# Kernel optimization log

Hardware: AMD Instinct MI355X
Metric: run time of the kernel (lower is better)

## Reference

```python
import jax, jax.numpy as jnp
import numpy as np

SELECT_SIZE = 64
SM_SCALE = 0.07216878364870322  # 192 ** -0.5
V_HEAD_DIM = 128


def setup_inputs() -> dict:
    key = jax.random.key(0)
    k1, k2, k3, k4 = jax.random.split(key, 4)
    B, S, Hq, G, TOPK = 4, 2048, 16, 4, 16
    T = B * S
    NB = S // SELECT_SIZE  # 32 blocks per sequence
    q = jax.random.normal(k1, (T, Hq, 192), dtype=jnp.float32)
    k = jax.random.normal(k2, (T, Hq, 192), dtype=jnp.float32)
    v = jax.random.normal(k3, (T, Hq, V_HEAD_DIM), dtype=jnp.float32)
    idx = jax.random.randint(k4, (T, G, TOPK), 0, NB, dtype=jnp.int32)
    # guarantee block 0 is always selected so every causal row has >=1 valid key
    idx = idx.at[..., 0].set(0)
    idx = jnp.sort(idx, axis=-1)
    return {"q": q, "k": k, "v": v, "selected_indices": idx,
            "batch_size": B, "seq_len": S}


def reference(q, k, v, selected_indices, batch_size, seq_len):
    B, S = batch_size, seq_len
    Hq = q.shape[1]
    G = selected_indices.shape[1]
    Hg = Hq // G  # query heads per selection-score group
    nb = (S + SELECT_SIZE - 1) // SELECT_SIZE
    dv = v.shape[-1]

    # un-ragged: B equal-length sequences
    qg = q.reshape(B, S, G, Hg, -1)
    kg = k.reshape(B, S, G, Hg, -1)
    vg = v.reshape(B, S, G, Hg, -1)
    idx = selected_indices.reshape(B, S, G, -1)

    # which KV blocks are selected for each (query position, group): [B,S,G,nb]
    allowed_blk = (idx[..., None] == jnp.arange(nb, dtype=idx.dtype)).any(axis=-2)
    blk_of_pos = jnp.arange(S) // SELECT_SIZE
    pos_ok = allowed_blk[..., blk_of_pos]  # [B, Tq, G, Skv]
    causal = jnp.arange(S)[:, None] >= jnp.arange(S)[None, :]
    mask = pos_ok & causal[None, :, None, :]          # [B, Tq, G, Skv]
    mask = mask.transpose(0, 2, 1, 3)[:, :, None]      # [B, G, 1, Tq, Skv]

    scores = jnp.einsum('btghd,bsghd->bghts', qg, kg) * SM_SCALE
    scores = jnp.where(mask, scores, jnp.float32(-1e30))
    attn = jax.nn.softmax(scores, axis=-1)
    o = jnp.einsum('bghts,bsghd->btghd', attn, vg)
    return o.reshape(B * S, Hq * dv)
```

## Files before the change

### kernel.cpp

```cpp
#include <hip/hip_runtime.h>


typedef __attribute__((ext_vector_type(8))) _Float16 half8;
typedef __attribute__((ext_vector_type(4))) float f32x4;
typedef __attribute__((ext_vector_type(4))) unsigned int u32x4;

__device__ __forceinline__ half8 cvt8s(const float4* p, float s) {
  float4 a = p[0], b = p[1];
  half8 r;
  r[0] = (_Float16)(a.x * s); r[1] = (_Float16)(a.y * s);
  r[2] = (_Float16)(a.z * s); r[3] = (_Float16)(a.w * s);
  r[4] = (_Float16)(b.x * s); r[5] = (_Float16)(b.y * s);
  r[6] = (_Float16)(b.z * s); r[7] = (_Float16)(b.w * s);
  return r;
}

__device__ __forceinline__ void async16(const void* g, void* l) {
  __builtin_amdgcn_global_load_lds(
      (const __attribute__((address_space(1))) void*)g,
      (__attribute__((address_space(3))) void*)l, 16, 0, 0);
}

__device__ __forceinline__ f32x4 vmax4(f32x4 a, f32x4 b) {
  f32x4 r;
  r[0] = fmaxf(a[0], b[0]); r[1] = fmaxf(a[1], b[1]);
  r[2] = fmaxf(a[2], b[2]); r[3] = fmaxf(a[3], b[3]);
  return r;
}

__global__ __launch_bounds__(256) void kv_prep(const float* __restrict__ k,
                                               const float* __restrict__ v,
                                               _Float16* __restrict__ kf,
                                               _Float16* __restrict__ vf) {
  __shared__ _Float16 lbh[64 * 200];
  int blk = blockIdx.x;
  int bh = blk >> 5, kb = blk & 31;
  int b = bh >> 4, h = bh & 15;
  int tid = threadIdx.x;

  const float* ksrc = k + ((long)(b * 2048 + kb * 64) * 16 + h) * 192;
#pragma unroll
  for (int it = 0; it < 12; ++it) {
    int idx = it * 256 + tid;
    int kk = idx / 48, c4 = idx - kk * 48;
    float4 x = *(const float4*)(ksrc + (long)kk * 3072 + c4 * 4);
    int s = ((kk >> 2) & 3) * 16 + ((kk >> 4) << 2) + (kk & 3);
    _Float16* d = &lbh[s * 200 + c4 * 4];
    d[0] = (_Float16)x.x; d[1] = (_Float16)x.y;
    d[2] = (_Float16)x.z; d[3] = (_Float16)x.w;
  }
  __syncthreads();
  _Float16* kdst = kf + (long)blk * 12288;
#pragma unroll
  for (int it = 0; it < 6; ++it) {
    int oct = it * 256 + tid;
    int frag = oct >> 6, lane = oct & 63;
    int ntile = frag / 6, kc = frag - ntile * 6;
    int s = ntile * 16 + (lane & 15);
    int d = kc * 32 + ((lane >> 4) << 3);
    *(half8*)(kdst + (long)oct * 8) = *(const half8*)(&lbh[s * 200 + d]);
  }
  __syncthreads();

  const float* vsrc = v + ((long)(b * 2048 + kb * 64) * 16 + h) * 128;
#pragma unroll
  for (int it = 0; it < 8; ++it) {
    int idx = it * 256 + tid;
    int kk = idx >> 5, c4 = idx & 31;
    float4 x = *(const float4*)(vsrc + (long)kk * 2048 + c4 * 4);
    _Float16* d = &lbh[kk * 140 + c4 * 4];
    d[0] = (_Float16)x.x; d[1] = (_Float16)x.y;
    d[2] = (_Float16)x.z; d[3] = (_Float16)x.w;
  }
  __syncthreads();
  _Float16* vdst = vf + (long)blk * 8192;
#pragma unroll
  for (int it = 0; it < 4; ++it) {
    int oct = it * 256 + tid;
    int frag = oct >> 6, lane = oct & 63;
    int n0 = frag >> 1, kc = frag & 1;
    int dv = n0 * 16 + (lane & 15);
    int kbase = kc * 32 + ((lane >> 4) << 3);
    half8 o;
#pragma unroll
    for (int j = 0; j < 8; ++j) o[j] = lbh[(kbase + j) * 140 + dv];
    *(half8*)(vdst + (long)oct * 8) = o;
  }
}

__global__ __launch_bounds__(256) void attn_main(const float* __restrict__ q,
                                                 const int* __restrict__ idx,
                                                 const _Float16* __restrict__ kf,
                                                 const _Float16* __restrict__ vf,
                                                 float* __restrict__ out) {
  constexpr float SCL = 0.07216878364870322f * 1.4426950408889634f;
  int id = (int)blockIdx.x;
  int qb = 31 - (id >> 6);
  int h = id & 15, b = (id >> 4) & 3, g = h >> 2;
  int tid = threadIdx.x;
  int w = tid >> 6, L = tid & 63;
  int Lm = L & 15, Lq = L >> 4;
  int m0 = w * 16;
  int t0 = b * 2048 + qb * 64;

  __shared__ __align__(16) char sh_kv[40960];
  __shared__ __align__(16) _Float16 Pbuf[4][16 * 72];
  __shared__ unsigned un_sh[4];
  char* lk = sh_kv;
  char* lv = sh_kv + 24576;

  half8 qa[6];
  const float* qrow = q + ((long)(t0 + m0 + Lm) * 16 + h) * 192;
#pragma unroll
  for (int c = 0; c < 6; ++c) qa[c] = cvt8s((const float4*)(qrow + c * 32 + Lq * 8), SCL);

  unsigned mrow = 0;
  {
    const int* ip = idx + ((long)(t0 + m0 + Lm) * 4 + g) * 16;
#pragma unroll
    for (int j = 0; j < 16; ++j) mrow |= (1u << ip[j]);
  }
  unsigned un = mrow;
#pragma unroll
  for (int o = 32; o; o >>= 1) un |= __shfl_xor(un, o, 64);
  if (L == 0) un_sh[w] = un;
  __syncthreads();
  unsigned bm = un_sh[0] | un_sh[1] | un_sh[2] | un_sh[3];

  f32x4 Oacc[8];
#pragma unroll
  for (int n0 = 0; n0 < 8; ++n0) Oacc[n0] = (f32x4){0.f, 0.f, 0.f, 0.f};
  float m_i = -1e30f, l_i = 0.f;

  const char* kfb = (const char*)(kf + (long)((b * 16 + h) * 32) * 12288);
  const char* vfb = (const char*)(vf + (long)((b * 16 + h) * 32) * 8192);
  _Float16* pw = &Pbuf[w][0];
  const half8* lkf = (const half8*)lk;
  const half8* lvf = (const half8*)lv;

  auto stage = [&](int kb) {
    const char* kg = kfb + (long)kb * 24576;
    const char* vg = vfb + (long)kb * 16384;
#pragma unroll
    for (int c = 0; c < 6; ++c) {
      int ch = w + c * 4;
      async16(kg + ch * 1024 + L * 16, lk + ch * 1024);
    }
#pragma unroll
    for (int c = 0; c < 4; ++c) {
      int ch = w + c * 4;
      async16(vg + ch * 1024 + L * 16, lv + ch * 1024);
    }
  };

  auto compute = [&](int kb, bool lastb) __attribute__((always_inline)) {
    f32x4 S[4];
#pragma unroll
    for (int nt = 0; nt < 4; ++nt) {
      f32x4 acc = {0.f, 0.f, 0.f, 0.f};
#pragma unroll
      for (int c = 0; c < 6; ++c)
        acc = __builtin_amdgcn_mfma_f32_16x16x32_f16(lkf[(nt * 6 + c) * 64 + L], qa[c], acc, 0, 0, 0);
      S[nt] = acc;
    }

    float p[4][4];
    float msel = ((mrow >> kb) & 1u) ? 1.0f : 0.0f;
    if (!lastb) {
      f32x4 t = vmax4(vmax4(S[0], S[1]), vmax4(S[2], S[3]));
      float rmax = fmaxf(fmaxf(t[0], t[1]), fmaxf(t[2], t[3]));
      rmax = fmaxf(rmax, __shfl_xor(rmax, 16));
      rmax = fmaxf(rmax, __shfl_xor(rmax, 32));
      if (__any(rmax > m_i)) {
        float mn = fmaxf(m_i, rmax);
        float av = __builtin_amdgcn_exp2f(m_i - mn);
        m_i = mn;
        l_i *= av;
#pragma unroll
        for (int n0 = 0; n0 < 8; ++n0) Oacc[n0] *= av;
      }
      float ps[4];
#pragma unroll
      for (int nt = 0; nt < 4; ++nt) {
        float s0 = 0.f, s1 = 0.f;
#pragma unroll
        for (int i = 0; i < 4; i += 2) {
          float a = __builtin_amdgcn_exp2f(S[nt][i] - m_i) * msel;
          float c = __builtin_amdgcn_exp2f(S[nt][i + 1] - m_i) * msel;
          p[nt][i] = a; p[nt][i + 1] = c;
          s0 += a; s1 += c;
        }
        ps[nt] = s0 + s1;
      }
      float psum = (ps[0] + ps[1]) + (ps[2] + ps[3]);
      psum += __shfl_xor(psum, 16);
      psum += __shfl_xor(psum, 32);
      l_i += psum;
    } else {
      float sc[4][4];
      float rmax = -1e30f;
#pragma unroll
      for (int nt = 0; nt < 4; ++nt)
#pragma unroll
        for (int i = 0; i < 4; ++i) {
          int key = Lq * 16 + nt * 4 + i;
          bool ok = (msel != 0.f) && (key <= m0 + Lm);
          float v = ok ? S[nt][i] : -1e30f;
          sc[nt][i] = v;
          rmax = fmaxf(rmax, v);
        }
      rmax = fmaxf(rmax, __shfl_xor(rmax, 16));
      rmax = fmaxf(rmax, __shfl_xor(rmax, 32));
      float mn = fmaxf(m_i, rmax);
      float av = __builtin_amdgcn_exp2f(m_i - mn);
      m_i = mn;
      float ps[4];
#pragma unroll
      for (int nt = 0; nt < 4; ++nt) {
        float s0 = 0.f;
#pragma unroll
        for (int i = 0; i < 4; ++i) {
          float a = __builtin_amdgcn_exp2f(sc[nt][i] - mn);
          p[nt][i] = a;
          s0 += a;
        }
        ps[nt] = s0;
      }
      float psum = (ps[0] + ps[1]) + (ps[2] + ps[3]);
      psum += __shfl_xor(psum, 16);
      psum += __shfl_xor(psum, 32);
      l_i = l_i * av + psum;
#pragma unroll
      for (int n0 = 0; n0 < 8; ++n0) Oacc[n0] *= av;
    }

    asm volatile("s_waitcnt lgkmcnt(0)" ::: "memory");
    u32x4 w0, w1;
    {
      auto c00 = __builtin_amdgcn_cvt_pkrtz(p[0][0], p[0][1]);
      auto c01 = __builtin_amdgcn_cvt_pkrtz(p[0][2], p[0][3]);
      auto c10 = __builtin_amdgcn_cvt_pkrtz(p[1][0], p[1][1]);
      auto c11 = __builtin_amdgcn_cvt_pkrtz(p[1][2], p[1][3]);
      auto c20 = __builtin_amdgcn_cvt_pkrtz(p[2][0], p[2][1]);
      auto c21 = __builtin_amdgcn_cvt_pkrtz(p[2][2], p[2][3]);
      auto c30 = __builtin_amdgcn_cvt_pkrtz(p[3][0], p[3][1]);
      auto c31 = __builtin_amdgcn_cvt_pkrtz(p[3][2], p[3][3]);
      w0[0] = __builtin_bit_cast(unsigned, c00); w0[1] = __builtin_bit_cast(unsigned, c01);
      w0[2] = __builtin_bit_cast(unsigned, c10); w0[3] = __builtin_bit_cast(unsigned, c11);
      w1[0] = __builtin_bit_cast(unsigned, c20); w1[1] = __builtin_bit_cast(unsigned, c21);
      w1[2] = __builtin_bit_cast(unsigned, c30); w1[3] = __builtin_bit_cast(unsigned, c31);
    }
    *(u32x4*)(pw + Lm * 72 + Lq * 16) = w0;
    *(u32x4*)(pw + Lm * 72 + Lq * 16 + 8) = w1;
    asm volatile("s_waitcnt lgkmcnt(0)" ::: "memory");

#pragma unroll
    for (int kc = 0; kc < 2; ++kc) {
      half8 pfr = *(const half8*)(pw + Lm * 72 + kc * 32 + Lq * 8);
#pragma unroll
      for (int n0 = 0; n0 < 8; ++n0)
        Oacc[n0] = __builtin_amdgcn_mfma_f32_16x16x32_f16(lvf[(n0 * 2 + kc) * 64 + L], pfr, Oacc[n0], 0, 0, 0);
    }
  };

  for (int kb = 0; kb < qb; ++kb) {
    if (!((bm >> kb) & 1u)) continue;
    stage(kb);
    asm volatile("s_waitcnt vmcnt(0)" ::: "memory");
    __syncthreads();
    if ((un >> kb) & 1u) compute(kb, false);
    __syncthreads();
  }
  if ((bm >> qb) & 1u) {
    stage(qb);
    asm volatile("s_waitcnt vmcnt(0)" ::: "memory");
    __syncthreads();
    if ((un >> qb) & 1u) compute(qb, true);
  }

  float inv = 1.f / l_i;
  float* orow = out + (long)(t0 + m0 + Lm) * 2048 + h * 128 + Lq * 4;
#pragma unroll
  for (int n0 = 0; n0 < 8; ++n0) {
    f32x4 o = Oacc[n0] * inv;
    *(f32x4*)(orow + n0 * 16) = o;
  }
}

extern "C" void kernel_launch(void* const* d_in, const int* in_sizes, int n_in,
                              void* d_out, int out_size, void* d_ws, size_t ws_size,
                              hipStream_t stream) {
  const float* q = (const float*)d_in[0];
  const float* k = (const float*)d_in[1];
  const float* v = (const float*)d_in[2];
  const int* idx = (const int*)d_in[3];
  _Float16* kf = (_Float16*)d_ws;
  _Float16* vf = kf + (size_t)2048 * 12288;
  float* out = (float*)d_out;
  kv_prep<<<2048, 256, 0, stream>>>(k, v, kf, vf);
  attn_main<<<2048, 256, 0, stream>>>(q, idx, kf, vf, out);
}
```

Measured before the change: 400.5 us.

## Alias P buffer into K LDS region and vectorize index and prep loads

The per-wave P staging buffer now reuses the K tile region of shared memory instead of a separate allocation, which lowers LDS use per block and may allow more resident blocks per CU. A barrier is added before the P writes so no wave overwrites K data another wave is still reading. Because that barrier sits inside the compute step, every wave must now run the compute step for each staged block, even when its own rows did not select that block. The selected-index mask is now built by loading each row's indices as int4, OR-reducing across the wave, and shuffling per-row masks, which removes a __syncthreads. The kv_prep kernel also packs its fp16 shared-memory stores into half4 writes.

```diff
diff --git a/kernel.cpp b/kernel.cpp
--- a/kernel.cpp
+++ b/kernel.cpp
@@ -2,6 +2,7 @@
 
 
 typedef __attribute__((ext_vector_type(8))) _Float16 half8;
+typedef __attribute__((ext_vector_type(4))) _Float16 half4;
 typedef __attribute__((ext_vector_type(4))) float f32x4;
 typedef __attribute__((ext_vector_type(4))) unsigned int u32x4;
 
@@ -32,7 +33,7 @@
                                                const float* __restrict__ v,
                                                _Float16* __restrict__ kf,
                                                _Float16* __restrict__ vf) {
-  __shared__ _Float16 lbh[64 * 200];
+  __shared__ __align__(16) _Float16 lbh[64 * 200];
   int blk = blockIdx.x;
   int bh = blk >> 5, kb = blk & 31;
   int b = bh >> 4, h = bh & 15;
@@ -45,9 +46,8 @@
     int kk = idx / 48, c4 = idx - kk * 48;
     float4 x = *(const float4*)(ksrc + (long)kk * 3072 + c4 * 4);
     int s = ((kk >> 2) & 3) * 16 + ((kk >> 4) << 2) + (kk & 3);
-    _Float16* d = &lbh[s * 200 + c4 * 4];
-    d[0] = (_Float16)x.x; d[1] = (_Float16)x.y;
-    d[2] = (_Float16)x.z; d[3] = (_Float16)x.w;
+    half4 hx = {(_Float16)x.x, (_Float16)x.y, (_Float16)x.z, (_Float16)x.w};
+    *(half4*)(&lbh[s * 200 + c4 * 4]) = hx;
   }
   __syncthreads();
   _Float16* kdst = kf + (long)blk * 12288;
@@ -68,9 +68,8 @@
     int idx = it * 256 + tid;
     int kk = idx >> 5, c4 = idx & 31;
     float4 x = *(const float4*)(vsrc + (long)kk * 2048 + c4 * 4);
-    _Float16* d = &lbh[kk * 140 + c4 * 4];
-    d[0] = (_Float16)x.x; d[1] = (_Float16)x.y;
-    d[2] = (_Float16)x.z; d[3] = (_Float16)x.w;
+    half4 hx = {(_Float16)x.x, (_Float16)x.y, (_Float16)x.z, (_Float16)x.w};
+    *(half4*)(&lbh[kk * 140 + c4 * 4]) = hx;
   }
   __syncthreads();
   _Float16* vdst = vf + (long)blk * 8192;
@@ -104,28 +103,28 @@
   int t0 = b * 2048 + qb * 64;
 
   __shared__ __align__(16) char sh_kv[40960];
-  __shared__ __align__(16) _Float16 Pbuf[4][16 * 72];
-  __shared__ unsigned un_sh[4];
   char* lk = sh_kv;
   char* lv = sh_kv + 24576;
+  _Float16* pw = (_Float16*)(lk + w * 2304);
 
   half8 qa[6];
   const float* qrow = q + ((long)(t0 + m0 + Lm) * 16 + h) * 192;
 #pragma unroll
   for (int c = 0; c < 6; ++c) qa[c] = cvt8s((const float4*)(qrow + c * 32 + Lq * 8), SCL);
 
-  unsigned mrow = 0;
+  unsigned rm = 0;
   {
-    const int* ip = idx + ((long)(t0 + m0 + Lm) * 4 + g) * 16;
-#pragma unroll
-    for (int j = 0; j < 16; ++j) mrow |= (1u << ip[j]);
-  }
-  unsigned un = mrow;
-#pragma unroll
-  for (int o = 32; o; o >>= 1) un |= __shfl_xor(un, o, 64);
-  if (L == 0) un_sh[w] = un;
-  __syncthreads();
-  unsigned bm = un_sh[0] | un_sh[1] | un_sh[2] | un_sh[3];
+    const int4* ip = (const int4*)(idx + ((long)(t0 + L) * 4 + g) * 16);
+#pragma unroll
+    for (int u = 0; u < 4; ++u) {
+      int4 iv = ip[u];
+      rm |= (1u << iv.x) | (1u << iv.y) | (1u << iv.z) | (1u << iv.w);
+    }
+  }
+  unsigned bm = rm;
+#pragma unroll
+  for (int o = 1; o < 64; o <<= 1) bm |= __shfl_xor(bm, o, 64);
+  unsigned mrow = __shfl(rm, m0 + Lm, 64);
 
   f32x4 Oacc[8];
 #pragma unroll
@@ -134,7 +133,6 @@
 
   const char* kfb = (const char*)(kf + (long)((b * 16 + h) * 32) * 12288);
   const char* vfb = (const char*)(vf + (long)((b * 16 + h) * 32) * 8192);
-  _Float16* pw = &Pbuf[w][0];
   const half8* lkf = (const half8*)lk;
   const half8* lvf = (const half8*)lv;
 
@@ -234,7 +232,6 @@
       for (int n0 = 0; n0 < 8; ++n0) Oacc[n0] *= av;
     }
 
-    asm volatile("s_waitcnt lgkmcnt(0)" ::: "memory");
     u32x4 w0, w1;
     {
       auto c00 = __builtin_amdgcn_cvt_pkrtz(p[0][0], p[0][1]);
@@ -250,6 +247,8 @@
       w1[0] = __builtin_bit_cast(unsigned, c20); w1[1] = __builtin_bit_cast(unsigned, c21);
       w1[2] = __builtin_bit_cast(unsigned, c30); w1[3] = __builtin_bit_cast(unsigned, c31);
     }
+
+    __syncthreads();
     *(u32x4*)(pw + Lm * 72 + Lq * 16) = w0;
     *(u32x4*)(pw + Lm * 72 + Lq * 16 + 8) = w1;
     asm volatile("s_waitcnt lgkmcnt(0)" ::: "memory");
@@ -268,14 +267,14 @@
     stage(kb);
     asm volatile("s_waitcnt vmcnt(0)" ::: "memory");
     __syncthreads();
-    if ((un >> kb) & 1u) compute(kb, false);
+    compute(kb, false);
     __syncthreads();
   }
   if ((bm >> qb) & 1u) {
     stage(qb);
     asm volatile("s_waitcnt vmcnt(0)" ::: "memory");
     __syncthreads();
-    if ((un >> qb) & 1u) compute(qb, true);
+    compute(qb, true);
   }
 
   float inv = 1.f / l_i;
```

Result: no change. 405.8 us (+1.3%).
